# Kernel tuning notes

Measured on AMD Instinct MI355X. Metric: run time of the kernel, lower is better.

## Reference

```python
import jax, jax.numpy as jnp
import numpy as np

ALPHA = 0.5
MODES = 12288  # == C*H*W, required by view_as in the original module
WIDTH = 512
B, C, H, W = 256, 3, 64, 64


def _linear_params(key, fan_in, fan_out):
    # torch.nn.Linear default init: U(-1/sqrt(fan_in), 1/sqrt(fan_in))
    k1, k2 = jax.random.split(key)
    s = 1.0 / np.sqrt(fan_in)
    Wm = jax.random.uniform(k1, (fan_in, fan_out), jnp.float32, -s, s)
    b = jax.random.uniform(k2, (fan_out,), jnp.float32, -s, s)
    return Wm, b


def setup_inputs() -> dict:
    key = jax.random.key(0)
    ks = jax.random.split(key, 6)
    x = jax.random.normal(ks[0], (B, C, H, W), jnp.float32)
    Ws1, bs1 = _linear_params(ks[1], MODES, WIDTH)   # spectral_operator
    Ws2, bs2 = _linear_params(ks[2], WIDTH, MODES)
    Wn1, bn1 = _linear_params(ks[3], MODES, WIDTH)   # neural_operator
    Wn2, bn2 = _linear_params(ks[4], WIDTH, WIDTH)
    Wn3, bn3 = _linear_params(ks[5], WIDTH, MODES)
    return {"x": x, "Ws1": Ws1, "bs1": bs1, "Ws2": Ws2, "bs2": bs2,
            "Wn1": Wn1, "bn1": bn1, "Wn2": Wn2, "bn2": bn2, "Wn3": Wn3, "bn3": bn3}


def _gl_fractional(f, alpha):
    """Grunwald-Letnikov fractional derivative on a 1-D signal sampled on
    t = linspace(0, 1, N):  D^a f[k] = h^{-a} * sum_{j<=k} w_j f[k-j],
    w_0 = 1, w_j = w_{j-1} * (j-1-a)/j  (i.e. (-1)^j * binom(a, j)).
    Implemented as an O(N log N) causal FFT convolution."""
    N = f.shape[0]
    j = jnp.arange(1, N, dtype=jnp.float32)
    w = jnp.concatenate([jnp.ones((1,), jnp.float32), jnp.cumprod((j - 1.0 - alpha) / j)])
    L = 2 * N  # >= N + N - 1 -> linear (causal) convolution
    conv = jnp.fft.irfft(jnp.fft.rfft(f, L) * jnp.fft.rfft(w, L), L)[:N]
    h = 1.0 / (N - 1)
    return conv * np.float32(h ** (-alpha))


def reference(x, Ws1, bs1, Ws2, bs2, Wn1, bn1, Wn2, bn2, Wn3, bn3):
    b, c, hh, ww = x.shape
    # (dead-code encoder branch of the original is omitted: its output x_frac
    #  is never used downstream)
    x_freq = jnp.fft.fft2(x, axes=(-2, -1))                 # complex64 (B,C,H,W)
    # _apply_fractional_operator: flattens the WHOLE real part into one signal
    fr = _gl_fractional(jnp.real(x_freq).reshape(-1), ALPHA).reshape(b, -1)  # (B, MODES)
    # spectral_operator: Linear -> ReLU -> Linear  (modes == C*H*W so [:modes] is identity)
    spec = jax.nn.relu(fr @ Ws1 + bs1) @ Ws2 + bs2          # (B, MODES)
    # neural_operator: Linear -> ReLU -> Linear -> ReLU -> Linear
    h1 = jax.nn.relu(spec @ Wn1 + bn1)
    h2 = jax.nn.relu(h1 @ Wn2 + bn2)
    proc = (h2 @ Wn3 + bn3).reshape(b, c, hh, ww)
    # complex(proc, 0) -> ifft2 -> real
    return jnp.real(jnp.fft.ifft2(proc.astype(jnp.complex64), axes=(-2, -1)))
```

## Files before the change

kernel.cpp:

```cpp
#include <hip/hip_runtime.h>
#include <hip/hip_bf16.h>

#define NTOT 3145728
#define NIMG 768
#define CTAPS 1024
#define NBAND 66

typedef __attribute__((ext_vector_type(8)))  short bf16x8;
typedef __attribute__((ext_vector_type(4)))  short bf16x4;
typedef __attribute__((ext_vector_type(8)))  unsigned short u16x8;
typedef __attribute__((ext_vector_type(4)))  unsigned short u16x4;
typedef __attribute__((ext_vector_type(4)))  float f32x4;
typedef __attribute__((ext_vector_type(16))) float f32x16;

__device__ inline unsigned short f2bf(float x) {
    unsigned u = __builtin_bit_cast(unsigned, x);
    u += 0x7fffu + ((u >> 16) & 1u);
    return (unsigned short)(u >> 16);
}
__device__ inline float bf2f(unsigned short u) {
    return __builtin_bit_cast(float, (unsigned)u << 16);
}
__device__ inline void split2(float v, unsigned short& hi, unsigned short& lo) {
    hi = f2bf(v);
    lo = f2bf(v - bf2f(hi));
}
__device__ inline bf16x8 ld2(const unsigned short* p) {
    bf16x4 a = *(const bf16x4*)p;
    bf16x4 b = *(const bf16x4*)(p + 4);
    bf16x8 r;
    #pragma unroll
    for (int i = 0; i < 4; ++i) { r[i] = a[i]; r[4 + i] = b[i]; }
    return r;
}

__global__ __launch_bounds__(1024)
void gen_tables(unsigned short* __restrict__ Tch, unsigned short* __restrict__ Tcl,
                unsigned short* __restrict__ Tsh, unsigned short* __restrict__ Tsl,
                unsigned short* __restrict__ Bth, unsigned short* __restrict__ Btl,
                unsigned short* __restrict__ fph, unsigned short* __restrict__ fpl)
{
    __shared__ float wsm[CTAPS];
    const int tid = threadIdx.x;
    const int bid = blockIdx.x;
    const float step = 6.28318530717958647692f / 64.0f;
    if (tid < 512) {
        int i = bid * 512 + tid;
        int p = i >> 6, q = i & 63;
        float ang = (float)((p * q) & 63) * step;
        unsigned short h, l;
        split2(cosf(ang), h, l); Tch[i] = h; Tcl[i] = l;
        split2(sinf(ang), h, l); Tsh[i] = h; Tsl[i] = l;
    }
    if (bid == 0) { fph[tid] = 0; fpl[tid] = 0; }
    if (tid < 64) {
        const int l = tid;
        float vals[16];
        float local = 1.0f;
        #pragma unroll
        for (int m = 0; m < 16; ++m) {
            int j = 16 * l + 1 + m;
            local *= ((float)j - 1.5f) / (float)j;
            vals[m] = local;
        }
        float scan = local;
        #pragma unroll
        for (int d = 1; d < 64; d <<= 1) {
            float o = __shfl_up(scan, (unsigned)d, 64);
            if (l >= d) scan *= o;
        }
        float prefix = __shfl_up(scan, 1u, 64);
        if (l == 0) prefix = 1.0f;
        const float s = sqrtf((float)(NTOT - 1));
        if (l == 0) wsm[0] = s;
        #pragma unroll
        for (int m = 0; m < 16; ++m) {
            int j = 16 * l + 1 + m;
            if (j < CTAPS) wsm[j] = prefix * vals[m] * s;
        }
    }
    __syncthreads();
    const int i0 = bid * 4224;
    for (int i = i0 + tid; i < i0 + 4224; i += 1024) {
        int d = (i >> 9) - 1, o = (i >> 4) & 31, u = i & 15;
        int j = 16 * d + o - u;
        unsigned short h = 0, l = 0;
        if (j >= 0 && j < CTAPS) split2(wsm[j], h, l);
        Bth[i] = h; Btl[i] = l;
    }
}

template<int INV>
__global__ __launch_bounds__(256)
void dft_mfma(const void* __restrict__ Xin, const unsigned short* __restrict__ Xlo_in,
              const unsigned short* __restrict__ Tch, const unsigned short* __restrict__ Tcl,
              const unsigned short* __restrict__ Tsh, const unsigned short* __restrict__ Tsl,
              void* __restrict__ Out, unsigned short* __restrict__ Out2)
{
    __shared__ __align__(16) unsigned short Xh[64 * 68], Xl[64 * 68];
    __shared__ __align__(16) unsigned short Chh[64 * 68], Cll[64 * 68];
    __shared__ __align__(16) unsigned short Shh[64 * 68], Sll[64 * 68];
    const int tid = threadIdx.x;
    const int img = blockIdx.x;
    {
        const int rr = tid >> 2, c0 = (tid & 3) * 16;
        const int lb = rr * 68 + c0;
        if (!INV) {
            const float* Xf = (const float*)Xin + (size_t)img * 4096 + rr * 64 + c0;
            #pragma unroll
            for (int i = 0; i < 4; ++i) {
                float4 v = *(const float4*)(Xf + 4 * i);
                float vv[4] = {v.x, v.y, v.z, v.w};
                #pragma unroll
                for (int k = 0; k < 4; ++k) {
                    unsigned short h, l; split2(vv[k], h, l);
                    Xh[lb + 4 * i + k] = h; Xl[lb + 4 * i + k] = l;
                }
            }
        } else {
            const unsigned short* Ph = (const unsigned short*)Xin + (size_t)img * 4096 + rr * 64 + c0;
            const unsigned short* Pl = Xlo_in + (size_t)img * 4096 + rr * 64 + c0;
            #pragma unroll
            for (int i = 0; i < 4; ++i) {
                *(ushort4*)&Xh[lb + 4 * i] = *(const ushort4*)(Ph + 4 * i);
                *(ushort4*)&Xl[lb + 4 * i] = *(const ushort4*)(Pl + 4 * i);
            }
        }
    }
    __syncthreads();

    const int lane = tid & 63, wv = tid >> 6;
    const int r = lane & 31, g = lane >> 5;
    const int q0 = (wv >> 1) * 32, r0 = (wv & 1) * 32;
    const int tA = (q0 + r) * 64;
    const int xB = (r0 + r) * 68;

    f32x16 a1, a2, a3;
    #pragma unroll
    for (int i = 0; i < 16; ++i) { a1[i] = 0.f; a2[i] = 0.f; a3[i] = 0.f; }
    #pragma unroll
    for (int ks = 0; ks < 4; ++ks) {
        const int ko = ks * 16 + 8 * g;
        bf16x8 xh = ld2(&Xh[xB + ko]);
        bf16x8 xl = ld2(&Xl[xB + ko]);
        bf16x8 th = *(const bf16x8*)&Tch[tA + ko];
        bf16x8 tl = *(const bf16x8*)&Tcl[tA + ko];
        a1 = __builtin_amdgcn_mfma_f32_32x32x16_bf16(th, xh, a1, 0, 0, 0);
        a2 = __builtin_amdgcn_mfma_f32_32x32x16_bf16(th, xl, a2, 0, 0, 0);
        a3 = __builtin_amdgcn_mfma_f32_32x32x16_bf16(tl, xh, a3, 0, 0, 0);
    }
    #pragma unroll
    for (int reg = 0; reg < 16; ++reg) {
        int qq = q0 + (reg & 3) + 8 * (reg >> 2) + 4 * g;
        unsigned short h, l; split2(a1[reg] + a2[reg] + a3[reg], h, l);
        Chh[qq * 68 + r0 + r] = h; Cll[qq * 68 + r0 + r] = l;
    }
    #pragma unroll
    for (int i = 0; i < 16; ++i) { a1[i] = 0.f; a2[i] = 0.f; a3[i] = 0.f; }
    #pragma unroll
    for (int ks = 0; ks < 4; ++ks) {
        const int ko = ks * 16 + 8 * g;
        bf16x8 xh = ld2(&Xh[xB + ko]);
        bf16x8 xl = ld2(&Xl[xB + ko]);
        bf16x8 th = *(const bf16x8*)&Tsh[tA + ko];
        bf16x8 tl = *(const bf16x8*)&Tsl[tA + ko];
        a1 = __builtin_amdgcn_mfma_f32_32x32x16_bf16(th, xh, a1, 0, 0, 0);
        a2 = __builtin_amdgcn_mfma_f32_32x32x16_bf16(th, xl, a2, 0, 0, 0);
        a3 = __builtin_amdgcn_mfma_f32_32x32x16_bf16(tl, xh, a3, 0, 0, 0);
    }
    #pragma unroll
    for (int reg = 0; reg < 16; ++reg) {
        int qq = q0 + (reg & 3) + 8 * (reg >> 2) + 4 * g;
        unsigned short h, l; split2(-(a1[reg] + a2[reg] + a3[reg]), h, l);
        Shh[qq * 68 + r0 + r] = h; Sll[qq * 68 + r0 + r] = l;
    }
    __syncthreads();

    #pragma unroll
    for (int i = 0; i < 16; ++i) { a1[i] = 0.f; a2[i] = 0.f; a3[i] = 0.f; }
    #pragma unroll
    for (int ks = 0; ks < 4; ++ks) {
        const int ko = ks * 16 + 8 * g;
        bf16x8 ch = ld2(&Chh[xB + ko]);
        bf16x8 cl = ld2(&Cll[xB + ko]);
        bf16x8 th = *(const bf16x8*)&Tch[tA + ko];
        bf16x8 tl = *(const bf16x8*)&Tcl[tA + ko];
        a1 = __builtin_amdgcn_mfma_f32_32x32x16_bf16(th, ch, a1, 0, 0, 0);
        a2 = __builtin_amdgcn_mfma_f32_32x32x16_bf16(th, cl, a2, 0, 0, 0);
        a3 = __builtin_amdgcn_mfma_f32_32x32x16_bf16(tl, ch, a3, 0, 0, 0);
        bf16x8 sh = ld2(&Shh[xB + ko]);
        bf16x8 sl = ld2(&Sll[xB + ko]);
        bf16x8 uh = *(const bf16x8*)&Tsh[tA + ko];
        bf16x8 ul = *(const bf16x8*)&Tsl[tA + ko];
        a1 = __builtin_amdgcn_mfma_f32_32x32x16_bf16(uh, sh, a1, 0, 0, 0);
        a2 = __builtin_amdgcn_mfma_f32_32x32x16_bf16(uh, sl, a2, 0, 0, 0);
        a3 = __builtin_amdgcn_mfma_f32_32x32x16_bf16(ul, sh, a3, 0, 0, 0);
    }
    #pragma unroll
    for (int reg = 0; reg < 16; ++reg) {
        int pp = q0 + (reg & 3) + 8 * (reg >> 2) + 4 * g;
        float v = a1[reg] + a2[reg] + a3[reg];
        size_t oi = (size_t)img * 4096 + (size_t)pp * 64 + r0 + r;
        if (INV) {
            ((float*)Out)[oi] = v * (1.0f / 4096.0f);
        } else {
            unsigned short h, l; split2(v, h, l);
            ((unsigned short*)Out)[oi] = h; Out2[oi] = l;
        }
    }
}

__global__ __launch_bounds__(256)
void conv_mfma(const unsigned short* __restrict__ fh, const unsigned short* __restrict__ fl,
               const unsigned short* __restrict__ Bth, const unsigned short* __restrict__ Btl,
               unsigned short* __restrict__ fr)
{
    __shared__ __align__(16) unsigned short Ah[5120], Al[5120];
    const int tid = threadIdx.x;
    const size_t tb0 = (size_t)blockIdx.x * 4096;
    {
        const unsigned short* sh = fh + tb0 - 1024;
        const unsigned short* sl = fl + tb0 - 1024;
        for (int gg = tid; gg < 640; gg += 256) {
            int off = (gg ^ ((gg >> 3) & 7)) << 3;
            *(bf16x8*)&Ah[off] = *(const bf16x8*)(sh + gg * 8);
            *(bf16x8*)&Al[off] = *(const bf16x8*)(sl + gg * 8);
        }
    }
    __syncthreads();

    const int lane = tid & 63;
    const int wv = tid >> 6;
    const int r = lane & 31, g = lane >> 5;
    const int bo = 16 * r + 8 * g;
    const int base_gg = 128 * (wv + 1) + 4 * r + g + 2;

    f32x16 a1, a2, a3;
    #pragma unroll
    for (int i = 0; i < 16; ++i) { a1[i] = 0.f; a2[i] = 0.f; a3[i] = 0.f; }

    const unsigned short* bhp = Bth + bo;
    const unsigned short* blp = Btl + bo;
    bf16x8 bh0 = *(const bf16x8*)(bhp);
    bf16x8 bl0 = *(const bf16x8*)(blp);
    bf16x8 bh1 = *(const bf16x8*)(bhp + 512);
    bf16x8 bl1 = *(const bf16x8*)(blp + 512);

    for (int dd = 0; dd < NBAND; dd += 2) {
        bf16x8 nh0, nl0, nh1, nl1;
        if (dd + 2 < NBAND) {
            nh0 = *(const bf16x8*)(bhp + 512 * (dd + 2));
            nl0 = *(const bf16x8*)(blp + 512 * (dd + 2));
            nh1 = *(const bf16x8*)(bhp + 512 * (dd + 3));
            nl1 = *(const bf16x8*)(blp + 512 * (dd + 3));
        }
        {
            int gg = base_gg - 2 * dd;
            int off = (gg ^ ((gg >> 3) & 7)) << 3;
            bf16x8 avh = *(const bf16x8*)&Ah[off];
            bf16x8 avl = *(const bf16x8*)&Al[off];
            a1 = __builtin_amdgcn_mfma_f32_32x32x16_bf16(avh, bh0, a1, 0, 0, 0);
            a2 = __builtin_amdgcn_mfma_f32_32x32x16_bf16(avl, bh0, a2, 0, 0, 0);
            a3 = __builtin_amdgcn_mfma_f32_32x32x16_bf16(avh, bl0, a3, 0, 0, 0);
        }
        {
            int gg = base_gg - 2 * (dd + 1);
            int off = (gg ^ ((gg >> 3) & 7)) << 3;
            bf16x8 avh = *(const bf16x8*)&Ah[off];
            bf16x8 avl = *(const bf16x8*)&Al[off];
            a1 = __builtin_amdgcn_mfma_f32_32x32x16_bf16(avh, bh1, a1, 0, 0, 0);
            a2 = __builtin_amdgcn_mfma_f32_32x32x16_bf16(avl, bh1, a2, 0, 0, 0);
            a3 = __builtin_amdgcn_mfma_f32_32x32x16_bf16(avh, bl1, a3, 0, 0, 0);
        }
        bh0 = nh0; bl0 = nl0; bh1 = nh1; bl1 = nl1;
    }

    const size_t tb = tb0 + 1024 * wv;
    #pragma unroll
    for (int reg = 0; reg < 16; ++reg) {
        int row = (reg & 3) + 8 * (reg >> 2) + 4 * g;
        fr[tb + 32 * row + r] = f2bf(a1[reg] + a2[reg] + a3[reg]);
    }
}

template<int MODE, int RELU, int BN>
__global__ __launch_bounds__(256)
void mfma_gemm(const unsigned short* __restrict__ A, const float* __restrict__ W,
               void* __restrict__ Out, const float* __restrict__ bias,
               int M, int N, int K, int kChunk, int nbn,
               unsigned short* __restrict__ Out2)
{
    constexpr int NE = (BN == 128) ? 8 : 4;
    constexpr int N4 = BN / 32;
    __shared__ unsigned short Bs[2][BN * 40];
    const int tid = threadIdx.x;
    const int id = blockIdx.x;
    const int gq = id >> 4, rr = id & 15;
    const int t  = gq * 8 + (rr & 7);
    const int bm = (rr >> 3) * 128;
    const int bn = (t % nbn) * BN;
    const int z  = t / nbn;
    const int kb0 = z * kChunk;
    const int nsteps = kChunk >> 5;

    const int lane = tid & 63;
    const int wv = tid >> 6;
    const int wr = (wv >> 1) * 64, wc = (wv & 1) * (BN / 2);
    const int l15 = lane & 15, l4 = lane >> 4;

    const int sn  = (BN == 128) ? (tid & 63) * 2 : (tid & 31) * 2;
    const int skq = (BN == 128) ? (tid >> 6) * 8 : (tid >> 5) * 4;

    f32x4 acc[4][N4];
    #pragma unroll
    for (int i = 0; i < 4; ++i)
        #pragma unroll
        for (int j = 0; j < N4; ++j)
            acc[i][j] = (f32x4){0.f, 0.f, 0.f, 0.f};

    const unsigned short* Arow = A + (size_t)(bm + wr + l15) * K + l4 * 8;
    float2 Rb0[NE], Rb1[NE];
    bf16x8 fa0[4], fa1[4];

#define LOADB(R, kb) { const float* Wp_ = W + (size_t)((kb) + skq) * N + bn + sn;         \
    _Pragma("unroll") for (int e = 0; e < NE; ++e) R[e] = *(const float2*)(Wp_ + (size_t)e * N); }
#define WRITEB(R, b) {                                                                    \
    if (BN == 128) {                                                                      \
        u16x8 p0_, p1_;                                                                   \
        _Pragma("unroll") for (int e = 0; e < NE; ++e) { p0_[e] = f2bf(R[e].x); p1_[e] = f2bf(R[e].y); } \
        *(u16x8*)&Bs[b][sn * 40 + skq]       = p0_;                                       \
        *(u16x8*)&Bs[b][(sn + 1) * 40 + skq] = p1_;                                       \
    } else {                                                                              \
        u16x4 p0_, p1_;                                                                   \
        _Pragma("unroll") for (int e = 0; e < NE; ++e) { p0_[e] = f2bf(R[e].x); p1_[e] = f2bf(R[e].y); } \
        *(u16x4*)&Bs[b][sn * 40 + skq]       = p0_;                                       \
        *(u16x4*)&Bs[b][(sn + 1) * 40 + skq] = p1_;                                       \
    } }
#define LOADA(F, kb) { _Pragma("unroll") for (int m4 = 0; m4 < 4; ++m4)                   \
    F[m4] = *(const bf16x8*)(Arow + (kb) + (size_t)m4 * 16 * K); }
#define RDB(fb, b) { _Pragma("unroll") for (int n4 = 0; n4 < N4; ++n4)                    \
    fb[n4] = *(const bf16x8*)&Bs[b][(wc + n4 * 16 + l15) * 40 + l4 * 8]; }
#define BARRIER_NODRAIN asm volatile("s_waitcnt lgkmcnt(0)\ns_barrier" ::: "memory")
#define MFMA_CL(fa_, fb_) { _Pragma("unroll") for (int m4 = 0; m4 < 4; ++m4)              \
    _Pragma("unroll") for (int n4 = 0; n4 < N4; ++n4)                                     \
        acc[m4][n4] = __builtin_amdgcn_mfma_f32_16x16x32_bf16(fa_[m4], fb_[n4], acc[m4][n4], 0, 0, 0); }

    LOADB(Rb0, kb0);
    WRITEB(Rb0, 0);
    LOADB(Rb1, kb0 + 32);
    LOADA(fa0, kb0);
    LOADA(fa1, kb0 + 32);
    __syncthreads();

    for (int s = 0; s < nsteps; s += 2) {
        const int kb = kb0 + s * 32;
        {
            bf16x8 fb[N4], acur[4];
            RDB(fb, 0);
            WRITEB(Rb1, 1);
            if (s + 2 < nsteps) LOADB(Rb0, kb + 64);
            #pragma unroll
            for (int m4 = 0; m4 < 4; ++m4) acur[m4] = fa0[m4];
            if (s + 2 < nsteps) LOADA(fa0, kb + 64);
            BARRIER_NODRAIN;
            MFMA_CL(acur, fb);
        }
        {
            bf16x8 fb[N4], acur[4];
            RDB(fb, 1);
            if (s + 2 < nsteps) WRITEB(Rb0, 0);
            if (s + 3 < nsteps) LOADB(Rb1, kb + 96);
            #pragma unroll
            for (int m4 = 0; m4 < 4; ++m4) acur[m4] = fa1[m4];
            if (s + 3 < nsteps) LOADA(fa1, kb + 96);
            BARRIER_NODRAIN;
            MFMA_CL(acur, fb);
        }
    }
#undef LOADB
#undef WRITEB
#undef LOADA
#undef RDB
#undef BARRIER_NODRAIN
#undef MFMA_CL

    #pragma unroll
    for (int m4 = 0; m4 < 4; ++m4)
        #pragma unroll
        for (int n4 = 0; n4 < N4; ++n4) {
            const int col = bn + wc + n4 * 16 + l15;
            const int row0 = bm + wr + m4 * 16 + l4 * 4;
            #pragma unroll
            for (int rg = 0; rg < 4; ++rg) {
                float v = acc[m4][n4][rg];
                const size_t oi = (size_t)(row0 + rg) * N + col;
                if (MODE == 0) {
                    ((float*)Out)[(size_t)z * M * N + oi] = v;
                } else {
                    v += bias[col];
                    if (RELU) v = fmaxf(v, 0.f);
                    if (MODE == 1) {
                        ((float*)Out)[oi] = v;
                    } else if (MODE == 2) {
                        ((unsigned short*)Out)[oi] = f2bf(v);
                    } else {
                        unsigned short h, l; split2(v, h, l);
                        ((unsigned short*)Out)[oi] = h; Out2[oi] = l;
                    }
                }
            }
        }
}

template<int RELU, int OUTBF>
__global__ __launch_bounds__(256)
void reduce_bias(const float* __restrict__ P, const float* __restrict__ bias,
                 void* __restrict__ C, int MN, int N, int S)
{
    const int idx4 = blockIdx.x * 256 + threadIdx.x;
    const int MN4 = MN >> 2;
    if (idx4 >= MN4) return;
    const float4* P4 = (const float4*)P;
    float4 a = P4[idx4];
    for (int zz = 1; zz < S; ++zz) {
        float4 b = P4[(size_t)zz * MN4 + idx4];
        a.x += b.x; a.y += b.y; a.z += b.z; a.w += b.w;
    }
    int n0 = (idx4 * 4) % N;
    a.x += bias[n0]; a.y += bias[n0 + 1]; a.z += bias[n0 + 2]; a.w += bias[n0 + 3];
    if (RELU) {
        a.x = fmaxf(a.x, 0.f); a.y = fmaxf(a.y, 0.f);
        a.z = fmaxf(a.z, 0.f); a.w = fmaxf(a.w, 0.f);
    }
    if (OUTBF) {
        ushort4 v = {f2bf(a.x), f2bf(a.y), f2bf(a.z), f2bf(a.w)};
        ((ushort4*)C)[idx4] = v;
    } else {
        ((float4*)C)[idx4] = a;
    }
}

extern "C" void kernel_launch(void* const* d_in, const int* in_sizes, int n_in,
                              void* d_out, int out_size, void* d_ws, size_t ws_size,
                              hipStream_t stream)
{
    const float* x   = (const float*)d_in[0];
    const float* Ws1 = (const float*)d_in[1];
    const float* bs1 = (const float*)d_in[2];
    const float* Ws2 = (const float*)d_in[3];
    const float* bs2 = (const float*)d_in[4];
    const float* Wn1 = (const float*)d_in[5];
    const float* bn1 = (const float*)d_in[6];
    const float* Wn2 = (const float*)d_in[7];
    const float* bn2 = (const float*)d_in[8];
    const float* Wn3 = (const float*)d_in[9];
    const float* bn3 = (const float*)d_in[10];
    float* out = (float*)d_out;

    char* p = (char*)d_ws;
    auto alloc = [&](size_t bytes) { char* q = p; p += (bytes + 255) & ~(size_t)255; return q; };
    unsigned short* Tch = (unsigned short*)alloc(8192);
    unsigned short* Tcl = (unsigned short*)alloc(8192);
    unsigned short* Tsh = (unsigned short*)alloc(8192);
    unsigned short* Tsl = (unsigned short*)alloc(8192);
    unsigned short* Bth = (unsigned short*)alloc((size_t)NBAND * 512 * 2);
    unsigned short* Btl = (unsigned short*)alloc((size_t)NBAND * 512 * 2);
    unsigned short* fhb = (unsigned short*)alloc((size_t)(1024 + NTOT) * 2);
    unsigned short* flb = (unsigned short*)alloc((size_t)(1024 + NTOT) * 2);
    unsigned short* fr   = (unsigned short*)alloc((size_t)NTOT * 2);
    unsigned short* spec = (unsigned short*)alloc((size_t)NTOT * 2);
    unsigned short* ph   = (unsigned short*)alloc((size_t)NTOT * 2);
    unsigned short* pl   = (unsigned short*)alloc((size_t)NTOT * 2);
    unsigned short* t1   = (unsigned short*)alloc(262144);
    unsigned short* h1   = (unsigned short*)alloc(262144);
    unsigned short* h2   = (unsigned short*)alloc(262144);
    float* part          = (float*)alloc((size_t)16 * 131072 * 4);

    gen_tables<<<8, 1024, 0, stream>>>(Tch, Tcl, Tsh, Tsl, Bth, Btl, fhb, flb);

    dft_mfma<0><<<NIMG, 256, 0, stream>>>(x, nullptr, Tch, Tcl, Tsh, Tsl,
                                          fhb + 1024, flb + 1024);

    conv_mfma<<<NTOT / 4096, 256, 0, stream>>>(fhb + 1024, flb + 1024, Bth, Btl, fr);

    mfma_gemm<0, 0, 64><<<256, 256, 0, stream>>>(fr, Ws1, part, nullptr,
                                                 256, 512, 12288, 768, 8, nullptr);
    reduce_bias<1, 1><<<128, 256, 0, stream>>>(part, bs1, t1, 131072, 512, 16);
    mfma_gemm<2, 0, 64><<<384, 256, 0, stream>>>(t1, Ws2, spec, bs2,
                                                 256, 12288, 512, 512, 192, nullptr);

    mfma_gemm<0, 0, 64><<<256, 256, 0, stream>>>(spec, Wn1, part, nullptr,
                                                 256, 512, 12288, 768, 8, nullptr);
    reduce_bias<1, 1><<<128, 256, 0, stream>>>(part, bn1, h1, 131072, 512, 16);
    mfma_gemm<0, 0, 64><<<128, 256, 0, stream>>>(h1, Wn2, part, nullptr,
                                                 256, 512, 512, 64, 8, nullptr);
    reduce_bias<1, 1><<<128, 256, 0, stream>>>(part, bn2, h2, 131072, 512, 8);
    mfma_gemm<3, 0, 64><<<384, 256, 0, stream>>>(h2, Wn3, ph, bn3,
                                                 256, 12288, 512, 512, 192, pl);

    dft_mfma<1><<<NIMG, 256, 0, stream>>>(ph, pl, Tch, Tcl, Tsh, Tsl, out, nullptr);
}
```

Measured before the change: 168.1 us.

## Deepen GEMM register prefetch to four stages and double split-K for wide-K GEMMs

Changes the GEMM main loop from a two-deep to a four-deep register prefetch of A fragments and B weight tiles, so global loads are issued further ahead of their MFMA use. It also halves the K chunk for the two K=12288 GEMMs (768 to 384), doubling their grid to 512 blocks and the split-K partial buffer to 32 slices, with the reduction adjusted to match. The aim is to hide more global memory latency and fill more CUs. The cost is higher register pressure, which may lower occupancy, plus twice the partial-sum traffic in the reduce kernels.

```diff
diff --git a/kernel.cpp b/kernel.cpp
--- a/kernel.cpp
+++ b/kernel.cpp
@@ -319,8 +319,8 @@
             acc[i][j] = (f32x4){0.f, 0.f, 0.f, 0.f};
 
     const unsigned short* Arow = A + (size_t)(bm + wr + l15) * K + l4 * 8;
-    float2 Rb0[NE], Rb1[NE];
-    bf16x8 fa0[4], fa1[4];
+    float2 Rb0[NE], Rb1[NE], Rb2[NE], Rb3[NE];
+    bf16x8 fa0[4], fa1[4], fa2[4], fa3[4];
 
 #define LOADB(R, kb) { const float* Wp_ = W + (size_t)((kb) + skq) * N + bn + sn;         \
     _Pragma("unroll") for (int e = 0; e < NE; ++e) R[e] = *(const float2*)(Wp_ + (size_t)e * N); }
@@ -344,38 +344,35 @@
 #define MFMA_CL(fa_, fb_) { _Pragma("unroll") for (int m4 = 0; m4 < 4; ++m4)              \
     _Pragma("unroll") for (int n4 = 0; n4 < N4; ++n4)                                     \
         acc[m4][n4] = __builtin_amdgcn_mfma_f32_16x16x32_bf16(fa_[m4], fb_[n4], acc[m4][n4], 0, 0, 0); }
+#define STEP(OFS, RBW, FAC) {                                                             \
+    const int s_ = s + (OFS);                                                             \
+    bf16x8 fb_[N4], acur_[4];                                                             \
+    RDB(fb_, (OFS) & 1);                                                                  \
+    if (s_ + 1 < nsteps) WRITEB(RBW, ((OFS) + 1) & 1);                                    \
+    if (s_ + 5 < nsteps) LOADB(RBW, kb0 + (s_ + 5) * 32);                                 \
+    _Pragma("unroll") for (int m4 = 0; m4 < 4; ++m4) acur_[m4] = FAC[m4];                 \
+    if (s_ + 4 < nsteps) LOADA(FAC, kb0 + (s_ + 4) * 32);                                 \
+    BARRIER_NODRAIN;                                                                      \
+    MFMA_CL(acur_, fb_);                                                                  \
+}
 
     LOADB(Rb0, kb0);
     WRITEB(Rb0, 0);
-    LOADB(Rb1, kb0 + 32);
+    if (1 < nsteps) LOADB(Rb1, kb0 + 32);
+    if (2 < nsteps) LOADB(Rb2, kb0 + 64);
+    if (3 < nsteps) LOADB(Rb3, kb0 + 96);
+    if (4 < nsteps) LOADB(Rb0, kb0 + 128);
     LOADA(fa0, kb0);
-    LOADA(fa1, kb0 + 32);
+    if (1 < nsteps) LOADA(fa1, kb0 + 32);
+    if (2 < nsteps) LOADA(fa2, kb0 + 64);
+    if (3 < nsteps) LOADA(fa3, kb0 + 96);
     __syncthreads();
 
-    for (int s = 0; s < nsteps; s += 2) {
-        const int kb = kb0 + s * 32;
-        {
-            bf16x8 fb[N4], acur[4];
-            RDB(fb, 0);
-            WRITEB(Rb1, 1);
-            if (s + 2 < nsteps) LOADB(Rb0, kb + 64);
-            #pragma unroll
-            for (int m4 = 0; m4 < 4; ++m4) acur[m4] = fa0[m4];
-            if (s + 2 < nsteps) LOADA(fa0, kb + 64);
-            BARRIER_NODRAIN;
-            MFMA_CL(acur, fb);
-        }
-        {
-            bf16x8 fb[N4], acur[4];
-            RDB(fb, 1);
-            if (s + 2 < nsteps) WRITEB(Rb0, 0);
-            if (s + 3 < nsteps) LOADB(Rb1, kb + 96);
-            #pragma unroll
-            for (int m4 = 0; m4 < 4; ++m4) acur[m4] = fa1[m4];
-            if (s + 3 < nsteps) LOADA(fa1, kb + 96);
-            BARRIER_NODRAIN;
-            MFMA_CL(acur, fb);
-        }
+    for (int s = 0; s < nsteps; s += 4) {
+        STEP(0, Rb1, fa0);
+        if (s + 1 < nsteps) STEP(1, Rb2, fa1);
+        if (s + 2 < nsteps) STEP(2, Rb3, fa2);
+        if (s + 3 < nsteps) STEP(3, Rb0, fa3);
     }
 #undef LOADB
 #undef WRITEB
@@ -383,6 +380,7 @@
 #undef RDB
 #undef BARRIER_NODRAIN
 #undef MFMA_CL
+#undef STEP
 
     #pragma unroll
     for (int m4 = 0; m4 < 4; ++m4)
@@ -474,7 +472,7 @@
     unsigned short* t1   = (unsigned short*)alloc(262144);
     unsigned short* h1   = (unsigned short*)alloc(262144);
     unsigned short* h2   = (unsigned short*)alloc(262144);
-    float* part          = (float*)alloc((size_t)16 * 131072 * 4);
+    float* part          = (float*)alloc((size_t)32 * 131072 * 4);
 
     gen_tables<<<8, 1024, 0, stream>>>(Tch, Tcl, Tsh, Tsl, Bth, Btl, fhb, flb);
 
@@ -483,15 +481,15 @@
 
     conv_mfma<<<NTOT / 4096, 256, 0, stream>>>(fhb + 1024, flb + 1024, Bth, Btl, fr);
 
-    mfma_gemm<0, 0, 64><<<256, 256, 0, stream>>>(fr, Ws1, part, nullptr,
-                                                 256, 512, 12288, 768, 8, nullptr);
-    reduce_bias<1, 1><<<128, 256, 0, stream>>>(part, bs1, t1, 131072, 512, 16);
+    mfma_gemm<0, 0, 64><<<512, 256, 0, stream>>>(fr, Ws1, part, nullptr,
+                                                 256, 512, 12288, 384, 8, nullptr);
+    reduce_bias<1, 1><<<128, 256, 0, stream>>>(part, bs1, t1, 131072, 512, 32);
     mfma_gemm<2, 0, 64><<<384, 256, 0, stream>>>(t1, Ws2, spec, bs2,
                                                  256, 12288, 512, 512, 192, nullptr);
 
-    mfma_gemm<0, 0, 64><<<256, 256, 0, stream>>>(spec, Wn1, part, nullptr,
-                                                 256, 512, 12288, 768, 8, nullptr);
-    reduce_bias<1, 1><<<128, 256, 0, stream>>>(part, bn1, h1, 131072, 512, 16);
+    mfma_gemm<0, 0, 64><<<512, 256, 0, stream>>>(spec, Wn1, part, nullptr,
+                                                 256, 512, 12288, 384, 8, nullptr);
+    reduce_bias<1, 1><<<128, 256, 0, stream>>>(part, bn1, h1, 131072, 512, 32);
     mfma_gemm<0, 0, 64><<<128, 256, 0, stream>>>(h1, Wn2, part, nullptr,
                                                  256, 512, 512, 64, 8, nullptr);
     reduce_bias<1, 1><<<128, 256, 0, stream>>>(part, bn2, h2, 131072, 512, 8);
```

Measured after the change: 181.5 us. +8.0%, slower.

## Pre-convert weights to blocked bf16 layout and drop LDS staging in GEMMs

Applied to the files above, without the earlier changes.

Adds a wconv kernel that converts all five fp32 weight matrices into bf16 once per call, transposed into 32-wide K-blocked tiles so each lane can load its MFMA B fragment directly from global memory. The GEMM kernel is rewritten to read these fragments straight into registers, removing shared-memory staging, per-tile fp32-to-bf16 conversion and the barriers. In exchange, every call reads all weights in fp32 and writes them again in bf16 (roughly 25M elements), which adds memory traffic to the timed path. Direct global fragment loads also lose the coalescing that LDS staging provided.

```diff
diff --git a/kernel.cpp b/kernel.cpp
--- a/kernel.cpp
+++ b/kernel.cpp
@@ -87,6 +87,45 @@
         unsigned short h = 0, l = 0;
         if (j >= 0 && j < CTAPS) split2(wsm[j], h, l);
         Bth[i] = h; Btl[i] = l;
+    }
+}
+
+__global__ __launch_bounds__(256)
+void wconv(const float* __restrict__ Ws1, const float* __restrict__ Ws2,
+           const float* __restrict__ Wn1, const float* __restrict__ Wn2,
+           const float* __restrict__ Wn3,
+           unsigned short* __restrict__ O1, unsigned short* __restrict__ O2,
+           unsigned short* __restrict__ O3, unsigned short* __restrict__ O4,
+           unsigned short* __restrict__ O5)
+{
+    __shared__ unsigned short tile[32][72];
+    int id = blockIdx.x;
+    const float* W; unsigned short* O; int N;
+    if (id < 3072)      { W = Ws1; O = O1; N = 512; }
+    else if (id < 6144) { W = Ws2; O = O2; N = 12288; id -= 3072; }
+    else if (id < 9216) { W = Wn1; O = O3; N = 512;   id -= 6144; }
+    else if (id < 9344) { W = Wn2; O = O4; N = 512;   id -= 9216; }
+    else                { W = Wn3; O = O5; N = 12288; id -= 9344; }
+    const int ng = N >> 6;
+    const int kp = id / ng, n0 = (id % ng) * 64;
+    const int t = threadIdx.x;
+    {
+        const int r = t >> 3, c0 = (t & 7) * 8;
+        const float* src = W + (size_t)(kp * 32 + r) * N + n0 + c0;
+        float4 v0 = *(const float4*)src;
+        float4 v1 = *(const float4*)(src + 4);
+        u16x8 o;
+        o[0] = f2bf(v0.x); o[1] = f2bf(v0.y); o[2] = f2bf(v0.z); o[3] = f2bf(v0.w);
+        o[4] = f2bf(v1.x); o[5] = f2bf(v1.y); o[6] = f2bf(v1.z); o[7] = f2bf(v1.w);
+        *(u16x8*)&tile[r][c0] = o;
+    }
+    __syncthreads();
+    {
+        const int n = t >> 2, sub = t & 3;
+        u16x8 v;
+        #pragma unroll
+        for (int j = 0; j < 8; ++j) v[j] = tile[sub * 8 + j][n];
+        *(u16x8*)&O[((size_t)kp * N + n0 + n) * 32 + sub * 8] = v;
     }
 }
 
@@ -283,111 +322,77 @@
     }
 }
 
-template<int MODE, int RELU, int BN>
+template<int MODE, int RELU>
 __global__ __launch_bounds__(256)
-void mfma_gemm(const unsigned short* __restrict__ A, const float* __restrict__ W,
-               void* __restrict__ Out, const float* __restrict__ bias,
-               int M, int N, int K, int kChunk, int nbn,
-               unsigned short* __restrict__ Out2)
-{
-    constexpr int NE = (BN == 128) ? 8 : 4;
-    constexpr int N4 = BN / 32;
-    __shared__ unsigned short Bs[2][BN * 40];
+void gemm_nb(const unsigned short* __restrict__ A, const unsigned short* __restrict__ Wt,
+             void* __restrict__ Out, const float* __restrict__ bias,
+             int M, int N, int K, int kChunk, int nbn,
+             unsigned short* __restrict__ Out2)
+{
     const int tid = threadIdx.x;
     const int id = blockIdx.x;
     const int gq = id >> 4, rr = id & 15;
     const int t  = gq * 8 + (rr & 7);
     const int bm = (rr >> 3) * 128;
-    const int bn = (t % nbn) * BN;
+    const int bn = (t % nbn) * 64;
     const int z  = t / nbn;
     const int kb0 = z * kChunk;
     const int nsteps = kChunk >> 5;
 
-    const int lane = tid & 63;
-    const int wv = tid >> 6;
-    const int wr = (wv >> 1) * 64, wc = (wv & 1) * (BN / 2);
+    const int lane = tid & 63, wv = tid >> 6;
+    const int wr = (wv >> 1) * 64, wc = (wv & 1) * 32;
     const int l15 = lane & 15, l4 = lane >> 4;
 
-    const int sn  = (BN == 128) ? (tid & 63) * 2 : (tid & 31) * 2;
-    const int skq = (BN == 128) ? (tid >> 6) * 8 : (tid >> 5) * 4;
-
-    f32x4 acc[4][N4];
+    f32x4 acc[4][2];
     #pragma unroll
     for (int i = 0; i < 4; ++i)
         #pragma unroll
-        for (int j = 0; j < N4; ++j)
+        for (int j = 0; j < 2; ++j)
             acc[i][j] = (f32x4){0.f, 0.f, 0.f, 0.f};
 
     const unsigned short* Arow = A + (size_t)(bm + wr + l15) * K + l4 * 8;
-    float2 Rb0[NE], Rb1[NE];
-    bf16x8 fa0[4], fa1[4];
-
-#define LOADB(R, kb) { const float* Wp_ = W + (size_t)((kb) + skq) * N + bn + sn;         \
-    _Pragma("unroll") for (int e = 0; e < NE; ++e) R[e] = *(const float2*)(Wp_ + (size_t)e * N); }
-#define WRITEB(R, b) {                                                                    \
-    if (BN == 128) {                                                                      \
-        u16x8 p0_, p1_;                                                                   \
-        _Pragma("unroll") for (int e = 0; e < NE; ++e) { p0_[e] = f2bf(R[e].x); p1_[e] = f2bf(R[e].y); } \
-        *(u16x8*)&Bs[b][sn * 40 + skq]       = p0_;                                       \
-        *(u16x8*)&Bs[b][(sn + 1) * 40 + skq] = p1_;                                       \
-    } else {                                                                              \
-        u16x4 p0_, p1_;                                                                   \
-        _Pragma("unroll") for (int e = 0; e < NE; ++e) { p0_[e] = f2bf(R[e].x); p1_[e] = f2bf(R[e].y); } \
-        *(u16x4*)&Bs[b][sn * 40 + skq]       = p0_;                                       \
-        *(u16x4*)&Bs[b][(sn + 1) * 40 + skq] = p1_;                                       \
-    } }
+    const unsigned short* Brow = Wt + ((size_t)(kb0 >> 5) * N + bn + wc + l15) * 32 + l4 * 8;
+    const size_t bstep = (size_t)N * 32;
+
+    bf16x8 fa0[4], fa1[4], fb0[2], fb1[2];
+
 #define LOADA(F, kb) { _Pragma("unroll") for (int m4 = 0; m4 < 4; ++m4)                   \
     F[m4] = *(const bf16x8*)(Arow + (kb) + (size_t)m4 * 16 * K); }
-#define RDB(fb, b) { _Pragma("unroll") for (int n4 = 0; n4 < N4; ++n4)                    \
-    fb[n4] = *(const bf16x8*)&Bs[b][(wc + n4 * 16 + l15) * 40 + l4 * 8]; }
-#define BARRIER_NODRAIN asm volatile("s_waitcnt lgkmcnt(0)\ns_barrier" ::: "memory")
+#define LOADFB(F, p) { F[0] = *(const bf16x8*)(Brow + (size_t)(p) * bstep);               \
+    F[1] = *(const bf16x8*)(Brow + (size_t)(p) * bstep + 512); }
 #define MFMA_CL(fa_, fb_) { _Pragma("unroll") for (int m4 = 0; m4 < 4; ++m4)              \
-    _Pragma("unroll") for (int n4 = 0; n4 < N4; ++n4)                                     \
+    _Pragma("unroll") for (int n4 = 0; n4 < 2; ++n4)                                      \
         acc[m4][n4] = __builtin_amdgcn_mfma_f32_16x16x32_bf16(fa_[m4], fb_[n4], acc[m4][n4], 0, 0, 0); }
 
-    LOADB(Rb0, kb0);
-    WRITEB(Rb0, 0);
-    LOADB(Rb1, kb0 + 32);
-    LOADA(fa0, kb0);
-    LOADA(fa1, kb0 + 32);
-    __syncthreads();
+    LOADA(fa0, kb0);    LOADFB(fb0, 0);
+    LOADA(fa1, kb0 + 32); LOADFB(fb1, 1);
 
     for (int s = 0; s < nsteps; s += 2) {
-        const int kb = kb0 + s * 32;
         {
-            bf16x8 fb[N4], acur[4];
-            RDB(fb, 0);
-            WRITEB(Rb1, 1);
-            if (s + 2 < nsteps) LOADB(Rb0, kb + 64);
+            bf16x8 ac[4], bc[2];
             #pragma unroll
-            for (int m4 = 0; m4 < 4; ++m4) acur[m4] = fa0[m4];
-            if (s + 2 < nsteps) LOADA(fa0, kb + 64);
-            BARRIER_NODRAIN;
-            MFMA_CL(acur, fb);
+            for (int m4 = 0; m4 < 4; ++m4) ac[m4] = fa0[m4];
+            bc[0] = fb0[0]; bc[1] = fb0[1];
+            if (s + 2 < nsteps) { LOADA(fa0, kb0 + (s + 2) * 32); LOADFB(fb0, s + 2); }
+            MFMA_CL(ac, bc);
         }
         {
-            bf16x8 fb[N4], acur[4];
-            RDB(fb, 1);
-            if (s + 2 < nsteps) WRITEB(Rb0, 0);
-            if (s + 3 < nsteps) LOADB(Rb1, kb + 96);
+            bf16x8 ac[4], bc[2];
             #pragma unroll
-            for (int m4 = 0; m4 < 4; ++m4) acur[m4] = fa1[m4];
-            if (s + 3 < nsteps) LOADA(fa1, kb + 96);
-            BARRIER_NODRAIN;
-            MFMA_CL(acur, fb);
-        }
-    }
-#undef LOADB
-#undef WRITEB
+            for (int m4 = 0; m4 < 4; ++m4) ac[m4] = fa1[m4];
+            bc[0] = fb1[0]; bc[1] = fb1[1];
+            if (s + 3 < nsteps) { LOADA(fa1, kb0 + (s + 3) * 32); LOADFB(fb1, s + 3); }
+            MFMA_CL(ac, bc);
+        }
+    }
 #undef LOADA
-#undef RDB
-#undef BARRIER_NODRAIN
+#undef LOADFB
 #undef MFMA_CL
 
     #pragma unroll
     for (int m4 = 0; m4 < 4; ++m4)
         #pragma unroll
-        for (int n4 = 0; n4 < N4; ++n4) {
+        for (int n4 = 0; n4 < 2; ++n4) {
             const int col = bn + wc + n4 * 16 + l15;
             const int row0 = bm + wr + m4 * 16 + l4 * 4;
             #pragma unroll
@@ -475,28 +480,36 @@
     unsigned short* h1   = (unsigned short*)alloc(262144);
     unsigned short* h2   = (unsigned short*)alloc(262144);
     float* part          = (float*)alloc((size_t)16 * 131072 * 4);
+    const size_t WB = (size_t)12288 * 512 * 2;
+    unsigned short* O1 = (unsigned short*)alloc(WB);
+    unsigned short* O2 = (unsigned short*)alloc(WB);
+    unsigned short* O3 = (unsigned short*)alloc(WB);
+    unsigned short* O4 = (unsigned short*)alloc((size_t)512 * 512 * 2);
+    unsigned short* O5 = (unsigned short*)alloc(WB);
 
     gen_tables<<<8, 1024, 0, stream>>>(Tch, Tcl, Tsh, Tsl, Bth, Btl, fhb, flb);
+
+    wconv<<<12416, 256, 0, stream>>>(Ws1, Ws2, Wn1, Wn2, Wn3, O1, O2, O3, O4, O5);
 
     dft_mfma<0><<<NIMG, 256, 0, stream>>>(x, nullptr, Tch, Tcl, Tsh, Tsl,
                                           fhb + 1024, flb + 1024);
 
     conv_mfma<<<NTOT / 4096, 256, 0, stream>>>(fhb + 1024, flb + 1024, Bth, Btl, fr);
 
-    mfma_gemm<0, 0, 64><<<256, 256, 0, stream>>>(fr, Ws1, part, nullptr,
-                                                 256, 512, 12288, 768, 8, nullptr);
+    gemm_nb<0, 0><<<256, 256, 0, stream>>>(fr, O1, part, nullptr,
+                                           256, 512, 12288, 768, 8, nullptr);
     reduce_bias<1, 1><<<128, 256, 0, stream>>>(part, bs1, t1, 131072, 512, 16);
-    mfma_gemm<2, 0, 64><<<384, 256, 0, stream>>>(t1, Ws2, spec, bs2,
-                                                 256, 12288, 512, 512, 192, nullptr);
-
-    mfma_gemm<0, 0, 64><<<256, 256, 0, stream>>>(spec, Wn1, part, nullptr,
-                                                 256, 512, 12288, 768, 8, nullptr);
+    gemm_nb<2, 0><<<384, 256, 0, stream>>>(t1, O2, spec, bs2,
+                                           256, 12288, 512, 512, 192, nullptr);
+
+    gemm_nb<0, 0><<<256, 256, 0, stream>>>(spec, O3, part, nullptr,
+                                           256, 512, 12288, 768, 8, nullptr);
     reduce_bias<1, 1><<<128, 256, 0, stream>>>(part, bn1, h1, 131072, 512, 16);
-    mfma_gemm<0, 0, 64><<<128, 256, 0, stream>>>(h1, Wn2, part, nullptr,
-                                                 256, 512, 512, 64, 8, nullptr);
+    gemm_nb<0, 0><<<128, 256, 0, stream>>>(h1, O4, part, nullptr,
+                                           256, 512, 512, 64, 8, nullptr);
     reduce_bias<1, 1><<<128, 256, 0, stream>>>(part, bn2, h2, 131072, 512, 8);
-    mfma_gemm<3, 0, 64><<<384, 256, 0, stream>>>(h2, Wn3, ph, bn3,
-                                                 256, 12288, 512, 512, 192, pl);
+    gemm_nb<3, 0><<<384, 256, 0, stream>>>(h2, O5, ph, bn3,
+                                           256, 12288, 512, 512, 192, pl);
 
     dft_mfma<1><<<NIMG, 256, 0, stream>>>(ph, pl, Tch, Tcl, Tsh, Tsl, out, nullptr);
 }
```

Result: slower. 184.8 us (+9.9%).
